# Optimization experiments

Measured on AMD Instinct MI355X. Metric: run time of the kernel, lower is better.

The kernel has to match this reference:

```python
import jax, jax.numpy as jnp
import numpy as np

N_NODES = 50000
N_EDGES = 1_600_000
D_IN = 512
D_OUT = 512


def setup_inputs() -> dict:
    key = jax.random.key(0)
    k_x, k_w, k_b, k_r, k_c, k_e = jax.random.split(key, 6)
    x = jax.random.normal(k_x, (N_NODES, D_IN), dtype=jnp.float32)
    stdv = 1.0 / np.sqrt(D_OUT)
    weight = jax.random.uniform(k_w, (D_IN, D_OUT), minval=-stdv, maxval=stdv, dtype=jnp.float32)
    bias = jax.random.uniform(k_b, (D_OUT,), minval=-stdv, maxval=stdv, dtype=jnp.float32)
    row = jax.random.randint(k_r, (N_EDGES,), 0, N_NODES, dtype=jnp.int32)
    col = jax.random.randint(k_c, (N_EDGES,), 0, N_NODES, dtype=jnp.int32)
    edge_weight = jax.random.uniform(k_e, (N_EDGES,), dtype=jnp.float32)
    return {"x": x, "weight": weight, "bias": bias, "row": row, "col": col, "edge_weight": edge_weight}


def reference(x, weight, bias, row, col, edge_weight):
    # support = X @ W   [N, D_OUT]
    support = x @ weight
    # spmm: out[i] = sum_{e: row[e]==i} edge_weight[e] * support[col[e]]
    msgs = edge_weight[:, None] * support[col]  # [E, D_OUT]
    out = jax.ops.segment_sum(msgs, row, num_segments=N_NODES)
    return out + bias
```

## Files before the change

kernel.cpp:

```cpp
#include <hip/hip_runtime.h>
#include <hip/hip_fp16.h>

#define D_DIM 512
#define BM 128
#define BN 128
#define BK 64

typedef _Float16 h8 __attribute__((ext_vector_type(8)));
typedef _Float16 h4 __attribute__((ext_vector_type(4)));
typedef float f32x4 __attribute__((ext_vector_type(4)));

#define LDS_PTR(p) ((__attribute__((address_space(3))) void*)(p))
#define GLB_PTR(p) ((const __attribute__((address_space(1))) void*)(p))


__global__ void k_zero(int* __restrict__ counts, int n) {
    int i = blockIdx.x * blockDim.x + threadIdx.x;
    if (i < n) counts[i] = 0;
}

__global__ void k_count(const int* __restrict__ row, int* __restrict__ counts, int E) {
    int e = blockIdx.x * blockDim.x + threadIdx.x;
    if (e < E) atomicAdd(&counts[row[e]], 1);
}

__global__ void k_scan_part(const int* __restrict__ counts, int* __restrict__ offsets,
                            int* __restrict__ bsum, int n) {
    __shared__ int s[1024];
    int t = threadIdx.x;
    int i = blockIdx.x * 1024 + t;
    int v = (i < n) ? counts[i] : 0;
    s[t] = v;
    __syncthreads();
    for (int off = 1; off < 1024; off <<= 1) {
        int x = (t >= off) ? s[t - off] : 0;
        __syncthreads();
        s[t] += x;
        __syncthreads();
    }
    if (i < n) offsets[i] = s[t] - v;
    if (t == 1023) bsum[blockIdx.x] = s[t];
}

__global__ void k_scan_top(int* __restrict__ bsum, int* __restrict__ offsets, int nb, int n) {
    int t = threadIdx.x;
    int v = (t < nb) ? bsum[t] : 0;
    int orig = v;
    for (int off = 1; off < 64; off <<= 1) {
        int u = __shfl_up(v, off, 64);
        if (t >= off) v += u;
    }
    if (t < nb) bsum[t] = v - orig;
    if (t == nb - 1) offsets[n] = v;
}

__global__ void k_scan_add(int* __restrict__ offsets, int* __restrict__ cursor,
                           const int* __restrict__ bsum, int n) {
    int i = blockIdx.x * 1024 + threadIdx.x;
    if (i < n) {
        int o = offsets[i] + bsum[blockIdx.x];
        offsets[i] = o;
        cursor[i] = o;
    }
}

__global__ void k_scatter(const int* __restrict__ row, const int* __restrict__ col,
                          const float* __restrict__ ew, int* __restrict__ cursor,
                          uint2* __restrict__ packed, int E) {
    int e = blockIdx.x * blockDim.x + threadIdx.x;
    if (e < E) {
        int r = row[e];
        int pos = atomicAdd(&cursor[r], 1);
        packed[pos] = make_uint2((unsigned)col[e], __float_as_uint(ew[e]));
    }
}


__global__ void k_wt(const float* __restrict__ w, _Float16* __restrict__ wt) {
    __shared__ _Float16 tile[32][33];
    int bx = blockIdx.x & 15, by = blockIdx.x >> 4;
    int tx = threadIdx.x & 31, ty = threadIdx.x >> 5;
    for (int r = 0; r < 32; r += 8)
        tile[ty + r][tx] = (_Float16)w[(size_t)(by * 32 + ty + r) * 512 + bx * 32 + tx];
    __syncthreads();
    for (int r = 0; r < 32; r += 8)
        wt[(size_t)(bx * 32 + ty + r) * 512 + by * 32 + tx] = tile[tx][ty + r];
}


__launch_bounds__(256)
__global__ void k_gemm(const float* __restrict__ x, const _Float16* __restrict__ wt,
                       _Float16* __restrict__ sup, int M) {
    __shared__ __align__(16) unsigned char As[BM * BK * 2];
    __shared__ __align__(16) unsigned char Bs[BN * BK * 2];

    const int t = threadIdx.x;
    const int lane = t & 63, w = t >> 6;
    const int wr = w >> 1, wc = w & 1;
    const int m0 = blockIdx.x * BM, n0 = blockIdx.y * BN;

    f32x4 acc[4][4] = {};

    const int ar_t = t >> 4;
    const int ac_t = (t & 15) * 4;
    const int bn_t = t >> 3;
    const int bk_sw = ((t & 7) * 16) ^ (((t >> 3) & 7) << 4);

    for (int kt = 0; kt < D_DIM / BK; ++kt) {
        const int k0 = kt * BK;
        for (int j = 0; j < 4; ++j) {
            int n = j * 32 + bn_t;
            const char* src = (const char*)(wt + (size_t)(n0 + n) * 512 + k0) + bk_sw;
            __builtin_amdgcn_global_load_lds(GLB_PTR(src), LDS_PTR(Bs + j * 4096 + t * 16),
                                             16, 0, 0);
        }
        for (int i = 0; i < 8; ++i) {
            int r = i * 16 + ar_t;
            int g = m0 + r;
            if (g >= M) g = M - 1;
            const float4 v = *(const float4*)(x + (size_t)g * 512 + k0 + ac_t);
            h4 hv;
            hv[0] = (_Float16)v.x; hv[1] = (_Float16)v.y;
            hv[2] = (_Float16)v.z; hv[3] = (_Float16)v.w;
            int addr = r * 128 + ((ac_t * 2) ^ ((r & 7) << 4));
            *(h4*)(As + addr) = hv;
        }
        __syncthreads();

        for (int ks = 0; ks < 2; ++ks) {
            h8 af[4], bf[4];
            const int kb = ks * 64 + ((lane >> 4) * 16);
#pragma unroll
            for (int mb = 0; mb < 4; ++mb) {
                int r = wr * 64 + mb * 16 + (lane & 15);
                af[mb] = *(const h8*)(As + r * 128 + (kb ^ ((r & 7) << 4)));
            }
#pragma unroll
            for (int nb = 0; nb < 4; ++nb) {
                int n = wc * 64 + nb * 16 + (lane & 15);
                bf[nb] = *(const h8*)(Bs + n * 128 + (kb ^ ((n & 7) << 4)));
            }
#pragma unroll
            for (int mb = 0; mb < 4; ++mb)
#pragma unroll
                for (int nb = 0; nb < 4; ++nb)
                    acc[mb][nb] = __builtin_amdgcn_mfma_f32_16x16x32_f16(
                        af[mb], bf[nb], acc[mb][nb], 0, 0, 0);
        }
        __syncthreads();
    }

    const int cr = (lane >> 4) * 4, cc = lane & 15;
#pragma unroll
    for (int mb = 0; mb < 4; ++mb) {
#pragma unroll
        for (int nb = 0; nb < 4; ++nb) {
            int gn = n0 + wc * 64 + nb * 16 + cc;
#pragma unroll
            for (int q = 0; q < 4; ++q) {
                int gm = m0 + wr * 64 + mb * 16 + cr + q;
                if (gm < M)
                    sup[(size_t)gm * 512 + gn] = (_Float16)acc[mb][nb][q];
            }
        }
    }
}


__global__ void k_spmm(const _Float16* __restrict__ sup, const uint2* __restrict__ packed,
                       const int* __restrict__ offsets, const float* __restrict__ bias,
                       float* __restrict__ out) {
    const int i = blockIdx.x;
    const int l = threadIdx.x;
    const int s0 = offsets[i], s1 = offsets[i + 1];

    float acc[8];
    const float4 b0 = *(const float4*)(bias + l * 8);
    const float4 b1 = *(const float4*)(bias + l * 8 + 4);
    acc[0] = b0.x; acc[1] = b0.y; acc[2] = b0.z; acc[3] = b0.w;
    acc[4] = b1.x; acc[5] = b1.y; acc[6] = b1.z; acc[7] = b1.w;

    for (int e = s0; e < s1; ++e) {
        uint2 p = packed[e];
        float wgt = __uint_as_float(p.y);
        h8 h = *(const h8*)(sup + (size_t)p.x * 512 + l * 8);
#pragma unroll
        for (int j = 0; j < 8; ++j) acc[j] += wgt * (float)h[j];
    }

    float4 o0 = {acc[0], acc[1], acc[2], acc[3]};
    float4 o1 = {acc[4], acc[5], acc[6], acc[7]};
    *(float4*)(out + (size_t)i * 512 + l * 8) = o0;
    *(float4*)(out + (size_t)i * 512 + l * 8 + 4) = o1;
}


extern "C" void kernel_launch(void* const* d_in, const int* in_sizes, int n_in,
                              void* d_out, int out_size, void* d_ws, size_t ws_size,
                              hipStream_t stream) {
    const float* x      = (const float*)d_in[0];
    const float* weight = (const float*)d_in[1];
    const float* bias   = (const float*)d_in[2];
    const int*   row    = (const int*)d_in[3];
    const int*   col    = (const int*)d_in[4];
    const float* ew     = (const float*)d_in[5];
    const int M = in_sizes[0] / D_DIM;
    const int E = in_sizes[3];
    float* out = (float*)d_out;

    char* ws = (char*)d_ws;
    size_t off = 0;
    auto alloc = [&](size_t bytes) {
        void* p = ws + off;
        off = (off + bytes + 255) & ~(size_t)255;
        return p;
    };
    _Float16* sup  = (_Float16*)alloc((size_t)M * D_DIM * 2);
    _Float16* wt   = (_Float16*)alloc((size_t)512 * 512 * 2);
    int* counts    = (int*)alloc((size_t)M * 4);
    int* offsets   = (int*)alloc((size_t)(M + 1) * 4);
    int* cursor    = (int*)alloc((size_t)M * 4);
    int* bsum      = (int*)alloc(64 * 4);
    uint2* packed  = (uint2*)alloc((size_t)E * 8);
    (void)ws_size; (void)n_in; (void)out_size;

    k_zero<<<(M + 255) / 256, 256, 0, stream>>>(counts, M);
    k_count<<<(E + 255) / 256, 256, 0, stream>>>(row, counts, E);
    const int SB = (M + 1023) / 1024;
    k_scan_part<<<SB, 1024, 0, stream>>>(counts, offsets, bsum, M);
    k_scan_top<<<1, 64, 0, stream>>>(bsum, offsets, SB, M);
    k_scan_add<<<SB, 1024, 0, stream>>>(offsets, cursor, bsum, M);
    k_scatter<<<(E + 255) / 256, 256, 0, stream>>>(row, col, ew, cursor, packed, E);

    k_wt<<<256, 256, 0, stream>>>(weight, wt);
    dim3 gg((M + BM - 1) / BM, D_DIM / BN);
    k_gemm<<<gg, 256, 0, stream>>>(x, wt, sup, M);

    k_spmm<<<M, 64, 0, stream>>>(sup, packed, offsets, bias, out);
}
```

Before: 649.6 us.

## Bucket edges by column chunk and sweep SpMM in phases for cache locality

Edges within each row are bucketed by column chunk (col>>11), using a 2D count, per-row scan and segment cursors. The SpMM now runs a fixed grid of waves, each owning 25 rows at strided indices. It sweeps column phases in lockstep so concurrent gathers of the support matrix hit a narrow band that fits in cache. The GEMM also moves to a 128x256 tile with an XCD-aware workgroup remap. The cost is extra preprocessing over a 32-slot-per-row count array and hardcoded sizes (2000 pairs x 25 rows = 50000 nodes) that only fit this node count.

```diff
diff --git a/kernel.cpp b/kernel.cpp
--- a/kernel.cpp
+++ b/kernel.cpp
@@ -3,8 +3,14 @@
 
 #define D_DIM 512
 #define BM 128
-#define BN 128
+#define BN 256
 #define BK 64
+
+#define NC_SHIFT 11
+#define NC_SLOT 32
+#define NPHASE 25
+#define NW_PAIRS 2000
+#define ROWS_PW 25
 
 typedef _Float16 h8 __attribute__((ext_vector_type(8)));
 typedef _Float16 h4 __attribute__((ext_vector_type(4)));
@@ -14,14 +20,36 @@
 #define GLB_PTR(p) ((const __attribute__((address_space(1))) void*)(p))
 
 
-__global__ void k_zero(int* __restrict__ counts, int n) {
+__global__ void k_zero2(int* __restrict__ counts2, int n) {
     int i = blockIdx.x * blockDim.x + threadIdx.x;
-    if (i < n) counts[i] = 0;
-}
-
-__global__ void k_count(const int* __restrict__ row, int* __restrict__ counts, int E) {
+    if (i < n) counts2[i] = 0;
+}
+
+__global__ void k_count2(const int* __restrict__ row, const int* __restrict__ col,
+                         int* __restrict__ counts2, int E) {
     int e = blockIdx.x * blockDim.x + threadIdx.x;
-    if (e < E) atomicAdd(&counts[row[e]], 1);
+    if (e < E) atomicAdd(&counts2[row[e] * NC_SLOT + (col[e] >> NC_SHIFT)], 1);
+}
+
+__global__ void k_rowscan(int* __restrict__ counts2, int* __restrict__ counts, int n) {
+    int r = blockIdx.x * blockDim.x + threadIdx.x;
+    if (r >= n) return;
+    int* p = counts2 + r * NC_SLOT;
+    int v[NC_SLOT];
+#pragma unroll
+    for (int i = 0; i < NC_SLOT / 4; ++i) {
+        int4 q = *(const int4*)(p + i * 4);
+        v[i * 4] = q.x; v[i * 4 + 1] = q.y; v[i * 4 + 2] = q.z; v[i * 4 + 3] = q.w;
+    }
+    int run = 0;
+#pragma unroll
+    for (int i = 0; i < NC_SLOT; ++i) { int t = v[i]; v[i] = run; run += t; }
+    counts[r] = run;
+#pragma unroll
+    for (int i = 0; i < NC_SLOT / 4; ++i) {
+        int4 q = {v[i * 4], v[i * 4 + 1], v[i * 4 + 2], v[i * 4 + 3]};
+        *(int4*)(p + i * 4) = q;
+    }
 }
 
 __global__ void k_scan_part(const int* __restrict__ counts, int* __restrict__ offsets,
@@ -54,24 +82,29 @@
     if (t == nb - 1) offsets[n] = v;
 }
 
-__global__ void k_scan_add(int* __restrict__ offsets, int* __restrict__ cursor,
-                           const int* __restrict__ bsum, int n) {
+__global__ void k_scan_add(int* __restrict__ offsets, const int* __restrict__ bsum, int n) {
     int i = blockIdx.x * 1024 + threadIdx.x;
-    if (i < n) {
-        int o = offsets[i] + bsum[blockIdx.x];
-        offsets[i] = o;
-        cursor[i] = o;
+    if (i < n) offsets[i] += bsum[blockIdx.x];
+}
+
+__global__ void k_seg(const int* __restrict__ offsets, const int* __restrict__ counts2,
+                      int* __restrict__ seg, int* __restrict__ cursor2, int n32) {
+    int i = blockIdx.x * blockDim.x + threadIdx.x;
+    if (i < n32) {
+        int v = offsets[i >> 5] + counts2[i];
+        seg[i] = v;
+        cursor2[i] = v;
     }
 }
 
 __global__ void k_scatter(const int* __restrict__ row, const int* __restrict__ col,
-                          const float* __restrict__ ew, int* __restrict__ cursor,
+                          const float* __restrict__ ew, int* __restrict__ cursor2,
                           uint2* __restrict__ packed, int E) {
     int e = blockIdx.x * blockDim.x + threadIdx.x;
     if (e < E) {
-        int r = row[e];
-        int pos = atomicAdd(&cursor[r], 1);
-        packed[pos] = make_uint2((unsigned)col[e], __float_as_uint(ew[e]));
+        int r = row[e], c = col[e];
+        int pos = atomicAdd(&cursor2[r * NC_SLOT + (c >> NC_SHIFT)], 1);
+        packed[pos] = make_uint2((unsigned)c, __float_as_uint(ew[e]));
     }
 }
 
@@ -90,16 +123,20 @@
 
 __launch_bounds__(256)
 __global__ void k_gemm(const float* __restrict__ x, const _Float16* __restrict__ wt,
-                       _Float16* __restrict__ sup, int M) {
+                       _Float16* __restrict__ sup, int M, int nwg) {
     __shared__ __align__(16) unsigned char As[BM * BK * 2];
     __shared__ __align__(16) unsigned char Bs[BN * BK * 2];
 
+    const int orig = blockIdx.x;
+    const int q = nwg >> 3, r = nwg & 7;
+    const int xcd = orig & 7, idx = orig >> 3;
+    const int wgid = (xcd < r ? xcd * (q + 1) : r * (q + 1) + (xcd - r) * q) + idx;
+    const int m0 = (wgid >> 1) * BM, n0 = (wgid & 1) * BN;
+
     const int t = threadIdx.x;
     const int lane = t & 63, w = t >> 6;
-    const int wr = w >> 1, wc = w & 1;
-    const int m0 = blockIdx.x * BM, n0 = blockIdx.y * BN;
-
-    f32x4 acc[4][4] = {};
+
+    f32x4 acc[8][4] = {};
 
     const int ar_t = t >> 4;
     const int ac_t = (t & 15) * 4;
@@ -108,40 +145,40 @@
 
     for (int kt = 0; kt < D_DIM / BK; ++kt) {
         const int k0 = kt * BK;
-        for (int j = 0; j < 4; ++j) {
+        for (int j = 0; j < 8; ++j) {
             int n = j * 32 + bn_t;
             const char* src = (const char*)(wt + (size_t)(n0 + n) * 512 + k0) + bk_sw;
             __builtin_amdgcn_global_load_lds(GLB_PTR(src), LDS_PTR(Bs + j * 4096 + t * 16),
                                              16, 0, 0);
         }
         for (int i = 0; i < 8; ++i) {
-            int r = i * 16 + ar_t;
-            int g = m0 + r;
+            int rr = i * 16 + ar_t;
+            int g = m0 + rr;
             if (g >= M) g = M - 1;
             const float4 v = *(const float4*)(x + (size_t)g * 512 + k0 + ac_t);
             h4 hv;
             hv[0] = (_Float16)v.x; hv[1] = (_Float16)v.y;
             hv[2] = (_Float16)v.z; hv[3] = (_Float16)v.w;
-            int addr = r * 128 + ((ac_t * 2) ^ ((r & 7) << 4));
+            int addr = rr * 128 + ((ac_t * 2) ^ ((rr & 7) << 4));
             *(h4*)(As + addr) = hv;
         }
         __syncthreads();
 
         for (int ks = 0; ks < 2; ++ks) {
-            h8 af[4], bf[4];
+            h8 af[8], bf[4];
             const int kb = ks * 64 + ((lane >> 4) * 16);
 #pragma unroll
-            for (int mb = 0; mb < 4; ++mb) {
-                int r = wr * 64 + mb * 16 + (lane & 15);
-                af[mb] = *(const h8*)(As + r * 128 + (kb ^ ((r & 7) << 4)));
+            for (int mb = 0; mb < 8; ++mb) {
+                int rr = mb * 16 + (lane & 15);
+                af[mb] = *(const h8*)(As + rr * 128 + (kb ^ ((rr & 7) << 4)));
             }
 #pragma unroll
             for (int nb = 0; nb < 4; ++nb) {
-                int n = wc * 64 + nb * 16 + (lane & 15);
+                int n = w * 64 + nb * 16 + (lane & 15);
                 bf[nb] = *(const h8*)(Bs + n * 128 + (kb ^ ((n & 7) << 4)));
             }
 #pragma unroll
-            for (int mb = 0; mb < 4; ++mb)
+            for (int mb = 0; mb < 8; ++mb)
 #pragma unroll
                 for (int nb = 0; nb < 4; ++nb)
                     acc[mb][nb] = __builtin_amdgcn_mfma_f32_16x16x32_f16(
@@ -152,46 +189,64 @@
 
     const int cr = (lane >> 4) * 4, cc = lane & 15;
 #pragma unroll
-    for (int mb = 0; mb < 4; ++mb) {
+    for (int mb = 0; mb < 8; ++mb) {
 #pragma unroll
         for (int nb = 0; nb < 4; ++nb) {
-            int gn = n0 + wc * 64 + nb * 16 + cc;
-#pragma unroll
-            for (int q = 0; q < 4; ++q) {
-                int gm = m0 + wr * 64 + mb * 16 + cr + q;
+            int gn = n0 + w * 64 + nb * 16 + cc;
+#pragma unroll
+            for (int qq = 0; qq < 4; ++qq) {
+                int gm = m0 + mb * 16 + cr + qq;
                 if (gm < M)
-                    sup[(size_t)gm * 512 + gn] = (_Float16)acc[mb][nb][q];
+                    sup[(size_t)gm * 512 + gn] = (_Float16)acc[mb][nb][qq];
             }
         }
     }
 }
 
 
+__launch_bounds__(256)
 __global__ void k_spmm(const _Float16* __restrict__ sup, const uint2* __restrict__ packed,
-                       const int* __restrict__ offsets, const float* __restrict__ bias,
+                       const int* __restrict__ seg, const float* __restrict__ bias,
                        float* __restrict__ out) {
-    const int i = blockIdx.x;
-    const int l = threadIdx.x;
-    const int s0 = offsets[i], s1 = offsets[i + 1];
-
-    float acc[8];
-    const float4 b0 = *(const float4*)(bias + l * 8);
-    const float4 b1 = *(const float4*)(bias + l * 8 + 4);
-    acc[0] = b0.x; acc[1] = b0.y; acc[2] = b0.z; acc[3] = b0.w;
-    acc[4] = b1.x; acc[5] = b1.y; acc[6] = b1.z; acc[7] = b1.w;
-
-    for (int e = s0; e < s1; ++e) {
-        uint2 p = packed[e];
-        float wgt = __uint_as_float(p.y);
-        h8 h = *(const h8*)(sup + (size_t)p.x * 512 + l * 8);
-#pragma unroll
-        for (int j = 0; j < 8; ++j) acc[j] += wgt * (float)h[j];
-    }
-
-    float4 o0 = {acc[0], acc[1], acc[2], acc[3]};
-    float4 o1 = {acc[4], acc[5], acc[6], acc[7]};
-    *(float4*)(out + (size_t)i * 512 + l * 8) = o0;
-    *(float4*)(out + (size_t)i * 512 + l * 8 + 4) = o1;
+    const int w = blockIdx.x * 4 + (threadIdx.x >> 6);
+    const int pair = w >> 1, half = w & 1, l = threadIdx.x & 63;
+    const int dcol = half * 256 + l * 4;
+    const _Float16* __restrict__ supl = sup + dcol;
+
+    const float4 b4 = *(const float4*)(bias + dcol);
+    f32x4 bias4 = {b4.x, b4.y, b4.z, b4.w};
+
+    f32x4 acc[ROWS_PW];
+    int s_[ROWS_PW];
+#pragma unroll
+    for (int rr = 0; rr < ROWS_PW; ++rr) {
+        acc[rr] = bias4;
+        s_[rr] = seg[(pair + rr * NW_PAIRS) * NC_SLOT];
+    }
+
+    for (int c = 0; c < NPHASE; ++c) {
+#pragma unroll
+        for (int rr = 0; rr < ROWS_PW; ++rr) {
+            const int e = seg[(pair + rr * NW_PAIRS) * NC_SLOT + c + 1];
+            int s = s_[rr];
+            for (; s < e; ++s) {
+                uint2 p = packed[s];
+                float wgt = __uint_as_float(p.y);
+                h4 h = *(const h4*)(supl + (size_t)p.x * 512);
+                acc[rr][0] += wgt * (float)h[0];
+                acc[rr][1] += wgt * (float)h[1];
+                acc[rr][2] += wgt * (float)h[2];
+                acc[rr][3] += wgt * (float)h[3];
+            }
+            s_[rr] = e;
+        }
+    }
+
+#pragma unroll
+    for (int rr = 0; rr < ROWS_PW; ++rr) {
+        float4 o = {acc[rr][0], acc[rr][1], acc[rr][2], acc[rr][3]};
+        *(float4*)(out + (size_t)(pair + rr * NW_PAIRS) * 512 + dcol) = o;
+    }
 }
 
 
@@ -219,22 +274,28 @@
     _Float16* wt   = (_Float16*)alloc((size_t)512 * 512 * 2);
     int* counts    = (int*)alloc((size_t)M * 4);
     int* offsets   = (int*)alloc((size_t)(M + 1) * 4);
-    int* cursor    = (int*)alloc((size_t)M * 4);
+    int* counts2   = (int*)alloc((size_t)M * NC_SLOT * 4);
+    int* seg       = (int*)alloc((size_t)M * NC_SLOT * 4);
+    int* cursor2   = (int*)alloc((size_t)M * NC_SLOT * 4);
     int* bsum      = (int*)alloc(64 * 4);
     uint2* packed  = (uint2*)alloc((size_t)E * 8);
     (void)ws_size; (void)n_in; (void)out_size;
 
-    k_zero<<<(M + 255) / 256, 256, 0, stream>>>(counts, M);
-    k_count<<<(E + 255) / 256, 256, 0, stream>>>(row, counts, E);
+    const int n32 = M * NC_SLOT;
+
+    k_zero2<<<(n32 + 255) / 256, 256, 0, stream>>>(counts2, n32);
+    k_count2<<<(E + 255) / 256, 256, 0, stream>>>(row, col, counts2, E);
+    k_rowscan<<<(M + 255) / 256, 256, 0, stream>>>(counts2, counts, M);
     const int SB = (M + 1023) / 1024;
     k_scan_part<<<SB, 1024, 0, stream>>>(counts, offsets, bsum, M);
     k_scan_top<<<1, 64, 0, stream>>>(bsum, offsets, SB, M);
-    k_scan_add<<<SB, 1024, 0, stream>>>(offsets, cursor, bsum, M);
-    k_scatter<<<(E + 255) / 256, 256, 0, stream>>>(row, col, ew, cursor, packed, E);
+    k_scan_add<<<SB, 1024, 0, stream>>>(offsets, bsum, M);
+    k_seg<<<(n32 + 255) / 256, 256, 0, stream>>>(offsets, counts2, seg, cursor2, n32);
+    k_scatter<<<(E + 255) / 256, 256, 0, stream>>>(row, col, ew, cursor2, packed, E);
 
     k_wt<<<256, 256, 0, stream>>>(weight, wt);
-    dim3 gg((M + BM - 1) / BM, D_DIM / BN);
-    k_gemm<<<gg, 256, 0, stream>>>(x, wt, sup, M);
-
-    k_spmm<<<M, 64, 0, stream>>>(sup, packed, offsets, bias, out);
-}
+    const int nwg = ((M + BM - 1) / BM) * (D_DIM / BN);
+    k_gemm<<<nwg, 256, 0, stream>>>(x, wt, sup, M, nwg);
+
+    k_spmm<<<NW_PAIRS / 2, 256, 0, stream>>>(sup, packed, seg, bias, out);
+}
```

New measurement: 2.151 ms. 231% more time.
